# Optimization experiments

Measured on AMD Instinct MI355X. Metric: run time of the kernel, lower is better.

Reference implementation:

```python
import jax, jax.numpy as jnp
import numpy as np

B, S, D, H = 2, 2048, 768, 12
DH = D // H  # 64


def setup_inputs() -> dict:
    key = jax.random.key(0)
    ks = jax.random.split(key, 6)
    sd = 1.0 / np.sqrt(D)
    x = jax.random.normal(ks[0], (B, S, 3 * D), dtype=jnp.float32)
    # causal additive mask: 1.0 where attention is disallowed (future positions)
    mask = jnp.triu(jnp.ones((S, S), dtype=jnp.float32), k=1)[None, None, :, :]
    return {
        "x": x,
        "mask": mask,
        "wq": jax.random.normal(ks[1], (D, D), dtype=jnp.float32) * sd,
        "bq": jnp.zeros((D,), dtype=jnp.float32),
        "wk": jax.random.normal(ks[2], (D, D), dtype=jnp.float32) * sd,
        "bk": jnp.zeros((D,), dtype=jnp.float32),
        "wv": jax.random.normal(ks[3], (D, D), dtype=jnp.float32) * sd,
        "bv": jnp.zeros((D,), dtype=jnp.float32),
        "wc": jax.random.normal(ks[4], (D, D), dtype=jnp.float32) * sd,
        "bc": jnp.zeros((D,), dtype=jnp.float32),
    }


def _split_heads(t):
    # [B, S, D] -> [B, H, S, DH]
    return t.reshape(B, S, H, DH).transpose(0, 2, 1, 3)


def reference(x, mask, wq, bq, wk, bk, wv, bv, wc, bc):
    xq, xk, xv = jnp.split(x, 3, axis=-1)
    q = _split_heads(xq @ wq + bq)
    k = _split_heads(xk @ wk + bk)
    v = _split_heads(xv @ wv + bv)
    scores = jnp.einsum("bhqd,bhkd->bhqk", q, k) / jnp.sqrt(jnp.float32(DH))
    scores = scores + mask * (-1e9)
    attn = jax.nn.softmax(scores, axis=-1)
    out = jnp.einsum("bhqk,bhkd->bhqd", attn, v)
    out = out.transpose(0, 2, 1, 3).reshape(B, S, D)  # merge heads
    return out @ wc + bc
```

## Files before the change

### kernel.cpp

```cpp
#include <hip/hip_runtime.h>
#include <math.h>

#define S_LEN   2048
#define D_MODEL 768
#define NH      12
#define DH      64
#define BATCH   2

typedef __attribute__((ext_vector_type(4)))  float f32x4;
typedef __attribute__((ext_vector_type(16))) float f32x16;
typedef __attribute__((ext_vector_type(8)))  short bf16x8;
typedef __attribute__((ext_vector_type(4)))  short short4v;

__device__ __forceinline__ short f2bf(float f) {
    union { float f; unsigned u; } v; v.f = f;
    unsigned r = (v.u + 0x7FFFu + ((v.u >> 16) & 1u)) >> 16;
    return (short)r;
}
__device__ __forceinline__ float bf2f(short s) {
    union { unsigned u; float f; } v; v.u = ((unsigned)(unsigned short)s) << 16;
    return v.f;
}
__device__ __forceinline__ unsigned cvt_pk_bf16(float lo, float hi) {
    unsigned r;
    asm("v_cvt_pk_bf16_f32 %0, %1, %2" : "=v"(r) : "v"(lo), "v"(hi));
    return r;
}
__device__ __forceinline__ void perm32swap(unsigned &a, unsigned &b) {
    asm("v_permlane32_swap_b32 %0, %1" : "+v"(a), "+v"(b));
}
__device__ __forceinline__ float exp2_fast(float x) {
    float r;
    asm("v_exp_f32 %0, %1" : "=v"(r) : "v"(x));
    return r;
}

#define GLOAD_LDS16(gp, lp)                                                     \
    __builtin_amdgcn_global_load_lds(                                           \
        (const __attribute__((address_space(1))) void*)(gp),                    \
        (__attribute__((address_space(3))) void*)(lp), 16, 0, 0)

__global__ __launch_bounds__(256) void convert_xw_kernel(
    const float* __restrict__ x, short* __restrict__ xb,
    const float* __restrict__ wq, const float* __restrict__ wk,
    const float* __restrict__ wv, const float* __restrict__ wc,
    short* __restrict__ wt)
{
    const int bid = blockIdx.x;
    const int t = threadIdx.x;
    if (bid < 4608) {
        const size_t i = ((size_t)bid * 256 + t) * 8;
        const f32x4 a = *(const f32x4*)(x + i);
        const f32x4 b = *(const f32x4*)(x + i + 4);
        bf16x8 r;
        r[0] = f2bf(a[0]); r[1] = f2bf(a[1]); r[2] = f2bf(a[2]); r[3] = f2bf(a[3]);
        r[4] = f2bf(b[0]); r[5] = f2bf(b[1]); r[6] = f2bf(b[2]); r[7] = f2bf(b[3]);
        *(bf16x8*)(xb + i) = r;
        return;
    }
    __shared__ float Ld[64][65];
    const int rem = bid - 4608;
    const int z  = rem / 144;
    const int yy = (rem % 144) / 12;
    const int xx = rem % 12;
    const float* W = (z == 0) ? wq : (z == 1) ? wk : (z == 2) ? wv : wc;
    short* dst = wt + (size_t)z * D_MODEL * D_MODEL;
    const int r0 = yy * 64;
    const int c0 = xx * 64;

#pragma unroll
    for (int i = 0; i < 4; ++i) {
        const int r = (t >> 4) + 16 * i;
        const int c = (t & 15) * 4;
        const float4 a = *(const float4*)(W + (size_t)(r0 + r) * D_MODEL + c0 + c);
        Ld[r][c + 0] = a.x; Ld[r][c + 1] = a.y; Ld[r][c + 2] = a.z; Ld[r][c + 3] = a.w;
    }
    __syncthreads();
#pragma unroll
    for (int i = 0; i < 4; ++i) {
        const int n = (t >> 4) + 16 * i;
        const int kq = (t & 15) * 4;
        short4v s4;
        s4[0] = f2bf(Ld[kq + 0][n]); s4[1] = f2bf(Ld[kq + 1][n]);
        s4[2] = f2bf(Ld[kq + 2][n]); s4[3] = f2bf(Ld[kq + 3][n]);
        *(short4v*)(dst + (size_t)(c0 + n) * D_MODEL + r0 + kq) = s4;
    }
}

template <int BM>
__device__ __forceinline__ void gemm_bt_body(
    const short* __restrict__ A, int lda,
    const short* __restrict__ Bt,
    const float* __restrict__ bias,
    void* __restrict__ C, int ldc, int out_mode)
{
    __shared__ __align__(16) char ldsA[BM * 128];
    __shared__ __align__(16) char ldsB[16384];

    const int t = threadIdx.x, lane = t & 63, w = t >> 6;
    const int l15 = lane & 15, l4 = lane >> 4;
    const int wr = w >> 1, wc = w & 1;
    constexpr int RB = BM / 32;

    const int l  = (int)blockIdx.x + (int)gridDim.x * (int)blockIdx.y;
    const int q8 = ((int)gridDim.x * (int)gridDim.y) >> 3;
    const int ls = (l & 7) * q8 + (l >> 3);
    const int row0 = (ls / (int)gridDim.x) * BM;
    const int col0 = (ls % (int)gridDim.x) * 128;

    const int srow = lane >> 3;
    const int sblk = (lane & 7) ^ srow;

    f32x4 acc[RB][4];
#pragma unroll
    for (int i = 0; i < RB; ++i)
#pragma unroll
        for (int j = 0; j < 4; ++j) acc[i][j] = (f32x4){0.f, 0.f, 0.f, 0.f};

    for (int kt = 0; kt < 12; ++kt) {
        __syncthreads();
#pragma unroll
        for (int i = 0; i < RB; ++i) {
            const int row = i * 32 + w * 8 + srow;
            GLOAD_LDS16(A + (size_t)(row0 + row) * lda + kt * 64 + sblk * 8,
                        ldsA + i * 4096 + w * 1024);
        }
#pragma unroll
        for (int i = 0; i < 4; ++i) {
            const int row = i * 32 + w * 8 + srow;
            GLOAD_LDS16(Bt + (size_t)(col0 + row) * D_MODEL + kt * 64 + sblk * 8,
                        ldsB + i * 4096 + w * 1024);
        }
        __syncthreads();

        bf16x8 af[RB][2], bfr[4][2];
#pragma unroll
        for (int rb = 0; rb < RB; ++rb) {
            const int r = wr * (BM / 2) + rb * 16 + l15;
#pragma unroll
            for (int c = 0; c < 2; ++c)
                af[rb][c] = *(const bf16x8*)(ldsA + r * 128 + (((c * 4 + l4) ^ (r & 7)) << 4));
        }
#pragma unroll
        for (int cb = 0; cb < 4; ++cb) {
            const int r = wc * 64 + cb * 16 + l15;
#pragma unroll
            for (int c = 0; c < 2; ++c)
                bfr[cb][c] = *(const bf16x8*)(ldsB + r * 128 + (((c * 4 + l4) ^ (r & 7)) << 4));
        }
        __builtin_amdgcn_s_setprio(1);
#pragma unroll
        for (int rb = 0; rb < RB; ++rb)
#pragma unroll
            for (int cb = 0; cb < 4; ++cb) {
                acc[rb][cb] = __builtin_amdgcn_mfma_f32_16x16x32_bf16(
                    af[rb][0], bfr[cb][0], acc[rb][cb], 0, 0, 0);
                acc[rb][cb] = __builtin_amdgcn_mfma_f32_16x16x32_bf16(
                    af[rb][1], bfr[cb][1], acc[rb][cb], 0, 0, 0);
            }
        __builtin_amdgcn_s_setprio(0);
    }

#pragma unroll
    for (int cb = 0; cb < 4; ++cb) {
        const int col = col0 + wc * 64 + cb * 16 + l15;
        const float bv = bias[col];
        if (out_mode == 2) {
            const int h  = col >> 6, dh = col & 63;
#pragma unroll
            for (int rb = 0; rb < RB; ++rb) {
                const int row = row0 + wr * (BM / 2) + rb * 16 + 4 * l4;
                const int b   = row >> 11, s0 = row & 2047;
                short4v s4;
                s4[0] = f2bf(acc[rb][cb][0] + bv);
                s4[1] = f2bf(acc[rb][cb][1] + bv);
                s4[2] = f2bf(acc[rb][cb][2] + bv);
                s4[3] = f2bf(acc[rb][cb][3] + bv);
                *(short4v*)((short*)C + ((size_t)((b * 12 + h) * 64 + dh)) * S_LEN + s0) = s4;
            }
        } else {
#pragma unroll
            for (int rb = 0; rb < RB; ++rb)
#pragma unroll
                for (int r = 0; r < 4; ++r) {
                    const int row = row0 + wr * (BM / 2) + rb * 16 + 4 * l4 + r;
                    const float val = acc[rb][cb][r] + bv;
                    if (out_mode == 1) ((short*)C)[(size_t)row * ldc + col] = f2bf(val);
                    else               ((float*)C)[(size_t)row * ldc + col] = val;
                }
        }
    }
}

__global__ __launch_bounds__(256) void qkv_gemm_kernel(
    const short* __restrict__ xb, const short* __restrict__ wt,
    const float* __restrict__ bq, const float* __restrict__ bk,
    const float* __restrict__ bv, short* __restrict__ qkv)
{
    const int which = blockIdx.z;
    const float* bias = (which == 0) ? bq : (which == 1) ? bk : bv;
    gemm_bt_body<64>(xb + which * D_MODEL, 3 * D_MODEL,
                     wt + (size_t)which * D_MODEL * D_MODEL, bias,
                     qkv + (size_t)which * BATCH * S_LEN * D_MODEL, D_MODEL,
                     (which == 2) ? 2 : 1);
}

__global__ __launch_bounds__(256) void proj_gemm_kernel(
    const short* __restrict__ att, const short* __restrict__ wct,
    const float* __restrict__ bc, float* __restrict__ out)
{
    gemm_bt_body<64>(att, D_MODEL, wct, bc, out, D_MODEL, 0);
}

__global__ __launch_bounds__(512, 4) void attn_mfma_kernel(
    const short* __restrict__ q, const short* __restrict__ k,
    const short* __restrict__ vt, short* __restrict__ o)
{
    __shared__ __align__(16) char bufK[2][2][8192];
    __shared__ __align__(16) char bufV[2][2][8192];
    __shared__ float mlx[2][128];

    const int t    = threadIdx.x;
    const int lane = t & 63;
    const int w    = t >> 6;
    const int g    = w >> 2;
    const int w4   = w & 3;
    const int l31  = lane & 31;
    const int hi   = lane >> 5;
    const int r7   = l31 & 7;

    const int h  = blockIdx.y;
    const int b  = blockIdx.z;
    const int bh = h + 12 * b;
    const int qt = (bh >= 16) ? (15 - (int)blockIdx.x) : (int)blockIdx.x;
    const int nt = qt + 1;

    const size_t base   = (size_t)b * (S_LEN * D_MODEL) + h * DH;
    const size_t vtbase = (size_t)bh * DH * S_LEN;
    const int q0 = qt * 128 + w4 * 32;

    bf16x8 qf[4];
    {
        const float qscale = 0.18033688f;
        const short* qp = q + base + (size_t)(q0 + l31) * D_MODEL + 8 * hi;
#pragma unroll
        for (int dc = 0; dc < 4; ++dc) {
            bf16x8 r = *(const bf16x8*)(qp + 16 * dc);
#pragma unroll
            for (int j = 0; j < 8; ++j) r[j] = f2bf(bf2f(r[j]) * qscale);
            qf[dc] = r;
        }
    }

    f32x16 oT[2];
    oT[0] = (f32x16)(0.f); oT[1] = (f32x16)(0.f);
    float mrun = -1e30f, lrun = 0.f;

    const int srow = lane >> 3;
    const int sblk = (lane & 7) ^ srow;

    {
        const int tk0 = g * nt;
#pragma unroll
        for (int i = 0; i < 2; ++i) {
            const int row = i * 32 + w4 * 8 + srow;
            GLOAD_LDS16(k  + base   + (size_t)(tk0 * 64 + row) * D_MODEL + sblk * 8,
                        bufK[g][0] + i * 4096 + w4 * 1024);
            GLOAD_LDS16(vt + vtbase + (size_t)row * S_LEN + tk0 * 64 + sblk * 8,
                        bufV[g][0] + i * 4096 + w4 * 1024);
        }
        __syncthreads();
    }

    for (int i = 0; i < nt; ++i) {
        const int cur = i & 1, nxt = cur ^ 1;
        const bool have_next = (i + 1 < nt);
        const int tk = g * nt + i;

        if (have_next) {
            const int tkn = tk + 1;
#pragma unroll
            for (int j = 0; j < 2; ++j) {
                const int row = j * 32 + w4 * 8 + srow;
                GLOAD_LDS16(k  + base   + (size_t)(tkn * 64 + row) * D_MODEL + sblk * 8,
                            bufK[g][nxt] + (size_t)(j * 4096 + w4 * 1024));
                GLOAD_LDS16(vt + vtbase + (size_t)row * S_LEN + tkn * 64 + sblk * 8,
                            bufV[g][nxt] + (size_t)(j * 4096 + w4 * 1024));
            }
        }

        if (tk * 64 <= q0 + 31) {
            f32x16 cS[2];
            __builtin_amdgcn_s_setprio(1);
#pragma unroll
            for (int s = 0; s < 2; ++s) {
                f32x16 acc = (f32x16)(0.f);
#pragma unroll
                for (int dc = 0; dc < 4; ++dc) {
                    const int row = 32 * s + l31;
                    const bf16x8 kf = *(const bf16x8*)(
                        bufK[g][cur] + row * 128 + (((unsigned)(32 * dc + 16 * hi)) ^ ((unsigned)r7 << 4)));
                    acc = __builtin_amdgcn_mfma_f32_32x32x16_bf16(kf, qf[dc], acc, 0, 0, 0);
                }
                cS[s] = acc;
            }
            __builtin_amdgcn_s_setprio(0);

            if (tk * 64 + 63 > q0) {
                const int qg = q0 + l31;
#pragma unroll
                for (int s = 0; s < 2; ++s)
#pragma unroll
                    for (int rg = 0; rg < 16; ++rg) {
                        const int key = tk * 64 + 32 * s + (rg & 3) + 8 * (rg >> 2) + 4 * hi;
                        if (key > qg) cS[s][rg] = -1e30f;
                    }
            }

            float pmax = -1e30f;
#pragma unroll
            for (int s = 0; s < 2; ++s)
#pragma unroll
                for (int rg = 0; rg < 16; ++rg) pmax = fmaxf(pmax, cS[s][rg]);
            pmax = fmaxf(pmax, __shfl_xor(pmax, 32));

            if (!__all(pmax - mrun <= 11.52f)) {
                const float mnew = fmaxf(mrun, pmax);
                const float corr = exp2_fast(mrun - mnew);
                lrun *= corr;
#pragma unroll
                for (int d0 = 0; d0 < 2; ++d0)
#pragma unroll
                    for (int rg = 0; rg < 16; ++rg) oT[d0][rg] *= corr;
                mrun = mnew;
            }
            float psum = 0.f;
#pragma unroll
            for (int s = 0; s < 2; ++s)
#pragma unroll
                for (int rg = 0; rg < 16; ++rg) {
                    const float e = exp2_fast(cS[s][rg] - mrun);
                    cS[s][rg] = e; psum += e;
                }
            psum += __shfl_xor(psum, 32);
            lrun += psum;

            bf16x8 pfrag[4];
#pragma unroll
            for (int s = 0; s < 2; ++s)
#pragma unroll
                for (int tt = 0; tt < 2; ++tt) {
                    unsigned a0 = cvt_pk_bf16(cS[s][8 * tt + 0], cS[s][8 * tt + 1]);
                    unsigned a1 = cvt_pk_bf16(cS[s][8 * tt + 2], cS[s][8 * tt + 3]);
                    unsigned b0 = cvt_pk_bf16(cS[s][8 * tt + 4], cS[s][8 * tt + 5]);
                    unsigned b1 = cvt_pk_bf16(cS[s][8 * tt + 6], cS[s][8 * tt + 7]);
                    perm32swap(a0, b0);
                    perm32swap(a1, b1);
                    union { unsigned u[4]; bf16x8 v8; } pk;
                    pk.u[0] = a0; pk.u[1] = a1; pk.u[2] = b0; pk.u[3] = b1;
                    pfrag[2 * s + tt] = pk.v8;
                }

            __builtin_amdgcn_s_setprio(1);
#pragma unroll
            for (int d0 = 0; d0 < 2; ++d0) {
                f32x16 acc = oT[d0];
#pragma unroll
                for (int c = 0; c < 4; ++c) {
                    const int row = 32 * d0 + l31;
                    const bf16x8 vf = *(const bf16x8*)(
                        bufV[g][cur] + row * 128 + (((unsigned)(32 * c + 16 * hi)) ^ ((unsigned)r7 << 4)));
                    acc = __builtin_amdgcn_mfma_f32_32x32x16_bf16(vf, pfrag[c], acc, 0, 0, 0);
                }
                oT[d0] = acc;
            }
            __builtin_amdgcn_s_setprio(0);
        }
        __syncthreads();
    }

    if (g == 1) {
        float* ex = (float*)(&bufK[0][0][0]) + w4 * 2048;
#pragma unroll
        for (int d0 = 0; d0 < 2; ++d0)
#pragma unroll
            for (int rg = 0; rg < 16; ++rg)
                ex[(d0 * 16 + rg) * 64 + lane] = oT[d0][rg];
        if (hi == 0) {
            mlx[0][w4 * 32 + l31] = mrun;
            mlx[1][w4 * 32 + l31] = lrun;
        }
    }
    __syncthreads();

    if (g == 0) {
        const int row = w4 * 32 + l31;
        const float m1  = mlx[0][row];
        const float l1v = mlx[1][row];
        const float M   = fmaxf(mrun, m1);
        const float a0  = exp2_fast(mrun - M);
        const float a1  = exp2_fast(m1 - M);
        const float inv = 1.f / (a0 * lrun + a1 * l1v);
        const float c0  = a0 * inv;
        const float c1  = a1 * inv;
        const float* ex = (const float*)(&bufK[0][0][0]) + w4 * 2048;

        short* orow = o + base + (size_t)(qt * 128 + row) * D_MODEL;
#pragma unroll
        for (int d0 = 0; d0 < 2; ++d0)
#pragma unroll
            for (int gg = 0; gg < 4; ++gg) {
                short4v s4;
#pragma unroll
                for (int j = 0; j < 4; ++j) {
                    const int rg = 4 * gg + j;
                    const float val = c0 * oT[d0][rg] + c1 * ex[(d0 * 16 + rg) * 64 + lane];
                    s4[j] = f2bf(val);
                }
                *(short4v*)(orow + 32 * d0 + 8 * gg + 4 * hi) = s4;
            }
    }
}

extern "C" void kernel_launch(void* const* d_in, const int* in_sizes, int n_in,
                              void* d_out, int out_size, void* d_ws, size_t ws_size,
                              hipStream_t stream)
{
    const float* x  = (const float*)d_in[0];
    const float* wq = (const float*)d_in[2];
    const float* bq = (const float*)d_in[3];
    const float* wk = (const float*)d_in[4];
    const float* bk = (const float*)d_in[5];
    const float* wv = (const float*)d_in[6];
    const float* bv = (const float*)d_in[7];
    const float* wc = (const float*)d_in[8];
    const float* bc = (const float*)d_in[9];
    float* out = (float*)d_out;

    const size_t nx  = (size_t)BATCH * S_LEN * 3 * D_MODEL;
    const size_t nw  = (size_t)D_MODEL * D_MODEL;
    const size_t nqv = (size_t)BATCH * S_LEN * D_MODEL;

    short* xb  = (short*)d_ws;
    short* wt  = xb + nx;
    short* qkv = wt + 4 * nw;
    short* att = qkv + 3 * nqv;

    dim3 blk(256);
    convert_xw_kernel<<<dim3(4608 + 576), blk, 0, stream>>>(x, xb, wq, wk, wv, wc, wt);
    qkv_gemm_kernel  <<<dim3(6, 64, 3), blk, 0, stream>>>(xb, wt, bq, bk, bv, qkv);
    attn_mfma_kernel <<<dim3(16, NH, BATCH), dim3(512), 0, stream>>>(
        qkv, qkv + nqv, qkv + 2 * nqv, att);
    proj_gemm_kernel <<<dim3(6, 64), blk, 0, stream>>>(att, wt + 3 * nw, bc, out);
}
```

Before: 90.26 us.

## Halve attention query tile to 64 rows with 256-thread blocks and balanced KV split

Restructures the attention kernel from 128-query tiles with 512 threads into 64-query tiles with 256 threads, doubling the grid. Each of the two wave groups now takes a ceil-half chunk of the causal KV tiles, with guards for groups that get fewer or no tiles, and results are merged at the end. The aim is more blocks for better CU occupancy and load balance on the causal triangle. In exchange, each K/V tile is loaded by twice as many blocks, and the launch bounds change register and occupancy targets.

Result: slower. 105.4 us (+16.8%).

```diff
diff --git a/kernel.cpp b/kernel.cpp
--- a/kernel.cpp
+++ b/kernel.cpp
@@ -212,19 +212,19 @@
     gemm_bt_body<64>(att, D_MODEL, wct, bc, out, D_MODEL, 0);
 }
 
-__global__ __launch_bounds__(512, 4) void attn_mfma_kernel(
+__global__ __launch_bounds__(256, 2) void attn_mfma_kernel(
     const short* __restrict__ q, const short* __restrict__ k,
     const short* __restrict__ vt, short* __restrict__ o)
 {
     __shared__ __align__(16) char bufK[2][2][8192];
     __shared__ __align__(16) char bufV[2][2][8192];
-    __shared__ float mlx[2][128];
+    __shared__ float mlx[2][64];
 
     const int t    = threadIdx.x;
     const int lane = t & 63;
     const int w    = t >> 6;
-    const int g    = w >> 2;
-    const int w4   = w & 3;
+    const int g    = w >> 1;
+    const int w2   = w & 1;
     const int l31  = lane & 31;
     const int hi   = lane >> 5;
     const int r7   = l31 & 7;
@@ -232,12 +232,15 @@
     const int h  = blockIdx.y;
     const int b  = blockIdx.z;
     const int bh = h + 12 * b;
-    const int qt = (bh >= 16) ? (15 - (int)blockIdx.x) : (int)blockIdx.x;
-    const int nt = qt + 1;
+    const int qb = (bh >= 16) ? (31 - (int)blockIdx.x) : (int)blockIdx.x;
+    const int nkt = qb + 1;
+    const int cpg = (nkt + 1) >> 1;
+    const int t0  = g * cpg;
+    int nld = nkt - t0; if (nld > cpg) nld = cpg; if (nld < 0) nld = 0;
 
     const size_t base   = (size_t)b * (S_LEN * D_MODEL) + h * DH;
     const size_t vtbase = (size_t)bh * DH * S_LEN;
-    const int q0 = qt * 128 + w4 * 32;
+    const int q0 = qb * 64 + w2 * 32;
 
     bf16x8 qf[4];
     {
@@ -259,37 +262,35 @@
     const int srow = lane >> 3;
     const int sblk = (lane & 7) ^ srow;
 
-    {
-        const int tk0 = g * nt;
-#pragma unroll
-        for (int i = 0; i < 2; ++i) {
-            const int row = i * 32 + w4 * 8 + srow;
-            GLOAD_LDS16(k  + base   + (size_t)(tk0 * 64 + row) * D_MODEL + sblk * 8,
-                        bufK[g][0] + i * 4096 + w4 * 1024);
-            GLOAD_LDS16(vt + vtbase + (size_t)row * S_LEN + tk0 * 64 + sblk * 8,
-                        bufV[g][0] + i * 4096 + w4 * 1024);
-        }
-        __syncthreads();
-    }
-
-    for (int i = 0; i < nt; ++i) {
+    if (nld > 0) {
+#pragma unroll
+        for (int j = 0; j < 4; ++j) {
+            const int row = j * 16 + w2 * 8 + srow;
+            GLOAD_LDS16(k  + base   + (size_t)(t0 * 64 + row) * D_MODEL + sblk * 8,
+                        bufK[g][0] + j * 2048 + w2 * 1024);
+            GLOAD_LDS16(vt + vtbase + (size_t)row * S_LEN + t0 * 64 + sblk * 8,
+                        bufV[g][0] + j * 2048 + w2 * 1024);
+        }
+    }
+    __syncthreads();
+
+    for (int i = 0; i < cpg; ++i) {
         const int cur = i & 1, nxt = cur ^ 1;
-        const bool have_next = (i + 1 < nt);
-        const int tk = g * nt + i;
-
-        if (have_next) {
+        const int tk = t0 + i;
+
+        if (i + 1 < nld) {
             const int tkn = tk + 1;
 #pragma unroll
-            for (int j = 0; j < 2; ++j) {
-                const int row = j * 32 + w4 * 8 + srow;
+            for (int j = 0; j < 4; ++j) {
+                const int row = j * 16 + w2 * 8 + srow;
                 GLOAD_LDS16(k  + base   + (size_t)(tkn * 64 + row) * D_MODEL + sblk * 8,
-                            bufK[g][nxt] + (size_t)(j * 4096 + w4 * 1024));
+                            bufK[g][nxt] + (size_t)(j * 2048 + w2 * 1024));
                 GLOAD_LDS16(vt + vtbase + (size_t)row * S_LEN + tkn * 64 + sblk * 8,
-                            bufV[g][nxt] + (size_t)(j * 4096 + w4 * 1024));
-            }
-        }
-
-        if (tk * 64 <= q0 + 31) {
+                            bufV[g][nxt] + (size_t)(j * 2048 + w2 * 1024));
+            }
+        }
+
+        if (i < nld && tk * 64 <= q0 + 31) {
             f32x16 cS[2];
             __builtin_amdgcn_s_setprio(1);
 #pragma unroll
@@ -380,21 +381,21 @@
     }
 
     if (g == 1) {
-        float* ex = (float*)(&bufK[0][0][0]) + w4 * 2048;
+        float* ex = (float*)(&bufK[0][0][0]) + w2 * 2048;
 #pragma unroll
         for (int d0 = 0; d0 < 2; ++d0)
 #pragma unroll
             for (int rg = 0; rg < 16; ++rg)
                 ex[(d0 * 16 + rg) * 64 + lane] = oT[d0][rg];
         if (hi == 0) {
-            mlx[0][w4 * 32 + l31] = mrun;
-            mlx[1][w4 * 32 + l31] = lrun;
+            mlx[0][w2 * 32 + l31] = mrun;
+            mlx[1][w2 * 32 + l31] = lrun;
         }
     }
     __syncthreads();
 
     if (g == 0) {
-        const int row = w4 * 32 + l31;
+        const int row = w2 * 32 + l31;
         const float m1  = mlx[0][row];
         const float l1v = mlx[1][row];
         const float M   = fmaxf(mrun, m1);
@@ -403,9 +404,9 @@
         const float inv = 1.f / (a0 * lrun + a1 * l1v);
         const float c0  = a0 * inv;
         const float c1  = a1 * inv;
-        const float* ex = (const float*)(&bufK[0][0][0]) + w4 * 2048;
-
-        short* orow = o + base + (size_t)(qt * 128 + row) * D_MODEL;
+        const float* ex = (const float*)(&bufK[0][0][0]) + w2 * 2048;
+
+        short* orow = o + base + (size_t)(qb * 64 + row) * D_MODEL;
 #pragma unroll
         for (int d0 = 0; d0 < 2; ++d0)
 #pragma unroll
@@ -449,7 +450,7 @@
     dim3 blk(256);
     convert_xw_kernel<<<dim3(4608 + 576), blk, 0, stream>>>(x, xb, wq, wk, wv, wc, wt);
     qkv_gemm_kernel  <<<dim3(6, 64, 3), blk, 0, stream>>>(xb, wt, bq, bk, bv, qkv);
-    attn_mfma_kernel <<<dim3(16, NH, BATCH), dim3(512), 0, stream>>>(
+    attn_mfma_kernel <<<dim3(32, NH, BATCH), blk, 0, stream>>>(
         qkv, qkv + nqv, qkv + 2 * nqv, att);
     proj_gemm_kernel <<<dim3(6, 64), blk, 0, stream>>>(att, wt + 3 * nw, bc, out);
 }
```
